# Kernel tuning notes

Hardware: AMD Instinct MI355X
Metric: run time of the kernel (lower is better)

The kernel has to match this reference:

```python
import jax, jax.numpy as jnp
import numpy as np
import math

N_HEADS = 16
D_EMBED = 1024
D_HEAD = D_EMBED // N_HEADS


def setup_inputs() -> dict:
    key = jax.random.key(0)
    ks = jax.random.split(key, 5)
    B, T = 4, 2048
    x = jax.random.normal(ks[0], (B, T, D_EMBED), dtype=jnp.float32)
    s_in = 1.0 / math.sqrt(D_EMBED)
    W_in = jax.random.normal(ks[1], (3 * D_EMBED, D_EMBED), dtype=jnp.float32) * s_in
    b_in = jax.random.normal(ks[2], (3 * D_EMBED,), dtype=jnp.float32) * s_in
    W_out = jax.random.normal(ks[3], (D_EMBED, D_EMBED), dtype=jnp.float32) * s_in
    b_out = jax.random.normal(ks[4], (D_EMBED,), dtype=jnp.float32) * s_in
    return {"x": x, "W_in": W_in, "b_in": b_in, "W_out": W_out, "b_out": b_out,
            "causal_mask": 1}


def reference(x, W_in, b_in, W_out, b_out, causal_mask):
    B, T, C = x.shape
    # in_proj: x @ W_in^T + b_in -> (B,T,3C), chunk into q,k,v
    qkv = jnp.einsum('btc,ec->bte', x, W_in) + b_in
    q, k, v = jnp.split(qkv, 3, axis=-1)
    # (B,T,H,Dh) -> (B,H,T,Dh)
    def heads(t):
        return t.reshape(B, T, N_HEADS, D_HEAD).transpose(0, 2, 1, 3)
    q, k, v = heads(q), heads(k), heads(v)
    scores = jnp.einsum('bhqd,bhkd->bhqk', q, k) / math.sqrt(D_HEAD)
    if causal_mask:
        mask = jnp.triu(jnp.ones((T, T), dtype=bool), k=1)  # True above diagonal
        scores = jnp.where(mask, -jnp.inf, scores)
    attn = jax.nn.softmax(scores, axis=-1)
    out = jnp.einsum('bhqk,bhkd->bhqd', attn, v)
    out = out.transpose(0, 2, 1, 3).reshape(B, T, C)
    out = jnp.einsum('btc,oc->bto', out, W_out) + b_out
    return out
```

## Files before the change

### kernel.cpp

```cpp
#include <hip/hip_runtime.h>
#include <hip/hip_bf16.h>

#define T_SEQ 2048
#define D_EMB 1024
#define NH    16
#define DH    64
#define NB    4
#define MROWS (NB * T_SEQ)
#define QKVN  (3 * D_EMB)

typedef __attribute__((ext_vector_type(8))) short bf16x8;
typedef __attribute__((ext_vector_type(4))) float f32x4;

__device__ __forceinline__ unsigned short f2bf(float f) {
  __hip_bfloat16 h = __float2bfloat16(f);
  return __builtin_bit_cast(unsigned short, h);
}

__device__ __forceinline__ void gload_lds16(const void* g, void* lds) {
  __builtin_amdgcn_global_load_lds(
      (const __attribute__((address_space(1))) void*)g,
      (__attribute__((address_space(3))) void*)lds, 16, 0, 0);
}

__global__ __launch_bounds__(256) void cvt_kernel(const float* __restrict__ in,
                                                  unsigned short* __restrict__ out,
                                                  int n4) {
  for (int i = blockIdx.x * 256 + threadIdx.x; i < n4; i += gridDim.x * 256) {
    const float4 v = reinterpret_cast<const float4*>(in)[i];
    ushort4 o;
    o.x = f2bf(v.x); o.y = f2bf(v.y); o.z = f2bf(v.z); o.w = f2bf(v.w);
    reinterpret_cast<ushort4*>(out)[i] = o;
  }
}

__global__ __launch_bounds__(256) void transposeV(const unsigned short* __restrict__ qkv,
                                                  unsigned short* __restrict__ vt) {
  __shared__ __align__(16) unsigned short Lt[64 * 72];
  const int tid = threadIdx.x;
  const int t0 = blockIdx.x * 64;
  const int bh = blockIdx.y;
  const int b  = bh >> 4;
  const int h  = bh & 15;
  const unsigned short* src = qkv + (size_t)(b * T_SEQ) * QKVN + 2 * D_EMB + h * DH;
#pragma unroll
  for (int g = 0; g < 2; ++g) {
    const int r = (tid >> 3) + g * 32;
    const int c = tid & 7;
    bf16x8 v = *reinterpret_cast<const bf16x8*>(src + (size_t)(t0 + r) * QKVN + c * 8);
    *reinterpret_cast<bf16x8*>(reinterpret_cast<char*>(Lt) + r * 144 + c * 16) = v;
  }
  __syncthreads();
#pragma unroll
  for (int g = 0; g < 2; ++g) {
    const int d  = (tid >> 3) + g * 32;
    const int tc = tid & 7;
    bf16x8 o;
#pragma unroll
    for (int j = 0; j < 8; ++j)
      ((unsigned short*)&o)[j] = Lt[(tc * 8 + j) * 72 + d];
    *reinterpret_cast<bf16x8*>(vt + ((size_t)bh * 64 + d) * T_SEQ + t0 + tc * 8) = o;
  }
}

template <int OUT_BF16>
__global__ __launch_bounds__(256) void gemm_bt(const unsigned short* __restrict__ A,
                                               const unsigned short* __restrict__ Bt,
                                               const float* __restrict__ bias,
                                               void* __restrict__ Cout,
                                               int M, int N, int K) {
  __shared__ __align__(16) unsigned short As[128 * 64];
  __shared__ __align__(16) unsigned short Bs[128 * 64];

  const int tid = threadIdx.x;
  const int w  = tid >> 6;
  const int l  = tid & 63;
  const int lr = l & 15;
  const int lg = l >> 4;

  const int gx   = gridDim.x;
  const int nwg  = gx * gridDim.y;
  const int orig = blockIdx.y * gx + blockIdx.x;
  const int swz  = (orig & 7) * (nwg >> 3) + (orig >> 3);
  const int bm = (swz / gx) * 128;
  const int bn = (swz % gx) * 128;

  const int wr = (w >> 1) * 64;
  const int wc = (w & 1) * 64;

  f32x4 acc[4][4];
#pragma unroll
  for (int i = 0; i < 4; ++i)
#pragma unroll
    for (int j = 0; j < 4; ++j) acc[i][j] = (f32x4){0.f, 0.f, 0.f, 0.f};

  const int cj = (l & 7) ^ (l >> 3);
  const unsigned short* Ab = A + (size_t)(bm + w * 32 + (l >> 3)) * K + cj * 8;
  const unsigned short* Bb = Bt + (size_t)(bn + w * 32 + (l >> 3)) * K + cj * 8;

  for (int kt = 0; kt < K; kt += 64) {
#pragma unroll
    for (int i = 0; i < 4; ++i) {
      gload_lds16(Ab + kt + (size_t)(i * 8) * K, &As[(w * 32 + i * 8) * 64]);
      gload_lds16(Bb + kt + (size_t)(i * 8) * K, &Bs[(w * 32 + i * 8) * 64]);
    }
    __syncthreads();

#pragma unroll
    for (int kk = 0; kk < 2; ++kk) {
      bf16x8 a[4], b[4];
#pragma unroll
      for (int mi = 0; mi < 4; ++mi) {
        const int R = wr + mi * 16 + lr;
        a[mi] = *reinterpret_cast<const bf16x8*>(
            &As[R * 64 + (((kk * 4 + lg) ^ (lr & 7)) << 3)]);
      }
#pragma unroll
      for (int ni = 0; ni < 4; ++ni) {
        const int R = wc + ni * 16 + lr;
        b[ni] = *reinterpret_cast<const bf16x8*>(
            &Bs[R * 64 + (((kk * 4 + lg) ^ (lr & 7)) << 3)]);
      }
#pragma unroll
      for (int mi = 0; mi < 4; ++mi)
#pragma unroll
        for (int ni = 0; ni < 4; ++ni)
          acc[mi][ni] = __builtin_amdgcn_mfma_f32_16x16x32_bf16(a[mi], b[ni], acc[mi][ni], 0, 0, 0);
    }
    __syncthreads();
  }

#pragma unroll
  for (int mi = 0; mi < 4; ++mi)
#pragma unroll
    for (int ni = 0; ni < 4; ++ni)
#pragma unroll
      for (int i = 0; i < 4; ++i) {
        const int row = bm + wr + mi * 16 + lg * 4 + i;
        const int col = bn + wc + ni * 16 + lr;
        const float v = acc[mi][ni][i] + bias[col];
        if (OUT_BF16)
          ((unsigned short*)Cout)[(size_t)row * N + col] = f2bf(v);
        else
          ((float*)Cout)[(size_t)row * N + col] = v;
      }
}

__global__ __launch_bounds__(512, 4) void attn_fwd(const unsigned short* __restrict__ qkv,
                                                   const unsigned short* __restrict__ vt,
                                                   unsigned short* __restrict__ attn_out,
                                                   const int* __restrict__ causal_flag) {
  __shared__ __align__(16) unsigned short Ks[64 * 64];
  __shared__ __align__(16) unsigned short Vt[64 * 64];
  __shared__ __align__(16) unsigned short Ps[8][16 * 64];

  const int tid = threadIdx.x;
  const int w  = tid >> 6;
  const int l  = tid & 63;
  const int lr = l & 15;
  const int lg = l >> 4;
  const int lk = lg * 8;
  const int bx = blockIdx.x;
  const int bh = blockIdx.y;
  const int b  = bh >> 4;
  const int h  = bh & 15;
  const int causal = causal_flag[0];

  const unsigned short* Qp  = qkv + (size_t)(b * T_SEQ) * QKVN + h * DH;
  const unsigned short* Kp  = Qp + D_EMB;
  const unsigned short* Vtp = vt + (size_t)bh * 64 * T_SEQ;

  const int scj = (l & 7) ^ (l >> 3);
  const int srr = l >> 3;

  for (int qq = 0; qq < 2; ++qq) {
    const int qt = qq ? (15 - bx) : bx;
    const int qbase = qt * 128;
    const int wrow0 = qbase + w * 16;

    bf16x8 qf[2];
#pragma unroll
    for (int ks = 0; ks < 2; ++ks) {
      bf16x8 v = *reinterpret_cast<const bf16x8*>(
          Qp + (size_t)(wrow0 + lr) * QKVN + ks * 32 + lk);
#pragma unroll
      for (int j = 0; j < 8; ++j) {
        const float f = __builtin_bit_cast(float, ((unsigned)(unsigned short)v[j]) << 16)
                        * 0.180336879f;
        v[j] = (short)(__builtin_bit_cast(unsigned, f) >> 16);
      }
      qf[ks] = v;
    }

    f32x4 oacc[4];
    float mrow = -INFINITY, lsum = 0.f;
#pragma unroll
    for (int di = 0; di < 4; ++di) oacc[di] = (f32x4){0.f, 0.f, 0.f, 0.f};

    const int nt = causal ? (qt * 2 + 2) : (T_SEQ / 64);

    for (int kb = 0; kb < nt; ++kb) {
      const int kbase = kb * 64;
      gload_lds16(Kp + (size_t)(kbase + w * 8 + srr) * QKVN + scj * 8,
                  &Ks[(w * 8) * 64]);
      gload_lds16(Vtp + (size_t)(w * 8 + srr) * T_SEQ + kbase + scj * 8,
                  &Vt[(w * 8) * 64]);
      __syncthreads();

      const bool live = !causal || (kbase <= wrow0 + 15);
      if (live) {
        f32x4 s[4];
#pragma unroll
        for (int ni = 0; ni < 4; ++ni) s[ni] = (f32x4){0.f, 0.f, 0.f, 0.f};
#pragma unroll
        for (int ks = 0; ks < 2; ++ks) {
          bf16x8 kf[4];
#pragma unroll
          for (int ni = 0; ni < 4; ++ni) {
            const int R = ni * 16 + lr;
            kf[ni] = *reinterpret_cast<const bf16x8*>(
                &Ks[R * 64 + (((ks * 4 + lg) ^ (lr & 7)) << 3)]);
          }
#pragma unroll
          for (int ni = 0; ni < 4; ++ni)
            s[ni] = __builtin_amdgcn_mfma_f32_16x16x32_bf16(kf[ni], qf[ks], s[ni], 0, 0, 0);
        }

        const bool mm = causal && (kbase + 63 > wrow0);
        const int qrow_rel = wrow0 + lr - kbase;
        float rmax = -INFINITY;
#pragma unroll
        for (int ni = 0; ni < 4; ++ni)
#pragma unroll
          for (int i = 0; i < 4; ++i) {
            float v = s[ni][i];
            if (mm && (ni * 16 + lg * 4 + i > qrow_rel)) v = -INFINITY;
            s[ni][i] = v;
            rmax = fmaxf(rmax, v);
          }
        rmax = fmaxf(rmax, __shfl_xor(rmax, 16));
        rmax = fmaxf(rmax, __shfl_xor(rmax, 32));
        const float mnew = fmaxf(mrow, rmax);
        const float alpha = exp2f(mrow - mnew);
        mrow = mnew;
        float psum = 0.f;
#pragma unroll
        for (int ni = 0; ni < 4; ++ni)
#pragma unroll
          for (int i = 0; i < 4; ++i) {
            const float p = exp2f(s[ni][i] - mnew);
            s[ni][i] = p;
            psum += p;
          }
        psum += __shfl_xor(psum, 16);
        psum += __shfl_xor(psum, 32);
        lsum = lsum * alpha + psum;

#pragma unroll
        for (int i = 0; i < 4; ++i) {
          const float a_bc = __shfl(alpha, (l & 48) | (lg * 4 + i));
#pragma unroll
          for (int di = 0; di < 4; ++di) oacc[di][i] *= a_bc;
        }

#pragma unroll
        for (int ni = 0; ni < 4; ++ni) {
          const unsigned lo = (unsigned)f2bf(s[ni][0]) | ((unsigned)f2bf(s[ni][1]) << 16);
          const unsigned hi = (unsigned)f2bf(s[ni][2]) | ((unsigned)f2bf(s[ni][3]) << 16);
          const int chunk = (ni * 2 + (lg >> 1)) ^ (lr & 7);
          uint2* dst = reinterpret_cast<uint2*>(
              reinterpret_cast<char*>(&Ps[w][0]) + lr * 128 + chunk * 16 + (lg & 1) * 8);
          *dst = make_uint2(lo, hi);
        }

#pragma unroll
        for (int ks2 = 0; ks2 < 2; ++ks2) {
          bf16x8 pf, vf[4];
          pf = *reinterpret_cast<const bf16x8*>(
              &Ps[w][lr * 64 + (((ks2 * 4 + lg) ^ (lr & 7)) << 3)]);
#pragma unroll
          for (int di = 0; di < 4; ++di) {
            const int R = di * 16 + lr;
            vf[di] = *reinterpret_cast<const bf16x8*>(
                &Vt[R * 64 + (((ks2 * 4 + lg) ^ (lr & 7)) << 3)]);
          }
#pragma unroll
          for (int di = 0; di < 4; ++di)
            oacc[di] = __builtin_amdgcn_mfma_f32_16x16x32_bf16(pf, vf[di], oacc[di], 0, 0, 0);
        }
      }
      __syncthreads();
    }

#pragma unroll
    for (int i = 0; i < 4; ++i) {
      const float ls = __shfl(lsum, (l & 48) | (lg * 4 + i));
      const float inv = 1.0f / ls;
#pragma unroll
      for (int di = 0; di < 4; ++di) {
        const int q = wrow0 + lg * 4 + i;
        const int d = di * 16 + lr;
        attn_out[(size_t)(b * T_SEQ + q) * D_EMB + h * DH + d] =
            f2bf(oacc[di][i] * inv);
      }
    }
  }
}

extern "C" void kernel_launch(void* const* d_in, const int* in_sizes, int n_in,
                              void* d_out, int out_size, void* d_ws, size_t ws_size,
                              hipStream_t stream) {
  const float* x     = (const float*)d_in[0];
  const float* W_in  = (const float*)d_in[1];
  const float* b_in  = (const float*)d_in[2];
  const float* W_out = (const float*)d_in[3];
  const float* b_out = (const float*)d_in[4];
  const int*   causal = (const int*)d_in[5];
  float* out = (float*)d_out;

  char* ws = (char*)d_ws;
  unsigned short* x_bf    = (unsigned short*)(ws);
  unsigned short* vt      = (unsigned short*)(ws);
  unsigned short* win_bf  = (unsigned short*)(ws + 16777216);
  unsigned short* wout_bf = (unsigned short*)(ws + 23068672);
  unsigned short* qkv     = (unsigned short*)(ws + 25165824);
  unsigned short* attn    = (unsigned short*)(ws + 75497472);

  cvt_kernel<<<2048, 256, 0, stream>>>(x, x_bf, (MROWS * D_EMB) / 4);
  cvt_kernel<<<2048, 256, 0, stream>>>(W_in, win_bf, (QKVN * D_EMB) / 4);
  cvt_kernel<<<1024, 256, 0, stream>>>(W_out, wout_bf, (D_EMB * D_EMB) / 4);

  gemm_bt<1><<<dim3(QKVN / 128, MROWS / 128), 256, 0, stream>>>(
      x_bf, win_bf, b_in, qkv, MROWS, QKVN, D_EMB);

  transposeV<<<dim3(T_SEQ / 64, NB * NH), 256, 0, stream>>>(qkv, vt);

  attn_fwd<<<dim3(8, NB * NH), 512, 0, stream>>>(qkv, vt, attn, causal);

  gemm_bt<0><<<dim3(D_EMB / 128, MROWS / 128), 256, 0, stream>>>(
      attn, wout_bf, b_out, out, MROWS, D_EMB, D_EMB);
}
```

Baseline: 296.3 us.

## Fuse both causal query tiles into one KV pass and skip unneeded rescales

Each block now processes its two paired query tiles (bx and 15-bx) together in a single KV loop. Every K/V tile is loaded into LDS once and shared by both, instead of running two separate sequential passes that reload the early tiles. It also adds a lazy max-rescale: the running max and output rescale are updated only when some row's new max exceeds the old one by more than 8 (log2 units). This costs extra registers for the second accumulator set and Q fragments, which may lower occupancy.

Result: slower. 339.0 us (+14.4%).

```diff
diff --git a/kernel.cpp b/kernel.cpp
--- a/kernel.cpp
+++ b/kernel.cpp
@@ -151,7 +151,7 @@
                                                    unsigned short* __restrict__ attn_out,
                                                    const int* __restrict__ causal_flag) {
   __shared__ __align__(16) unsigned short Ks[64 * 64];
-  __shared__ __align__(16) unsigned short Vt[64 * 64];
+  __shared__ __align__(16) unsigned short Vs[64 * 64];
   __shared__ __align__(16) unsigned short Ps[8][16 * 64];
 
   const int tid = threadIdx.x;
@@ -173,135 +173,161 @@
   const int scj = (l & 7) ^ (l >> 3);
   const int srr = l >> 3;
 
-  for (int qq = 0; qq < 2; ++qq) {
-    const int qt = qq ? (15 - bx) : bx;
-    const int qbase = qt * 128;
-    const int wrow0 = qbase + w * 16;
-
-    bf16x8 qf[2];
-#pragma unroll
-    for (int ks = 0; ks < 2; ++ks) {
+  const int qtA = bx, qtB = 15 - bx;
+  const int wrowA = qtA * 128 + w * 16;
+  const int wrowB = qtB * 128 + w * 16;
+
+  bf16x8 qfA[2], qfB[2];
+#pragma unroll
+  for (int ks = 0; ks < 2; ++ks) {
+#pragma unroll
+    for (int g = 0; g < 2; ++g) {
+      const int wr0 = g ? wrowB : wrowA;
       bf16x8 v = *reinterpret_cast<const bf16x8*>(
-          Qp + (size_t)(wrow0 + lr) * QKVN + ks * 32 + lk);
+          Qp + (size_t)(wr0 + lr) * QKVN + ks * 32 + lk);
 #pragma unroll
       for (int j = 0; j < 8; ++j) {
         const float f = __builtin_bit_cast(float, ((unsigned)(unsigned short)v[j]) << 16)
                         * 0.180336879f;
         v[j] = (short)(__builtin_bit_cast(unsigned, f) >> 16);
       }
-      qf[ks] = v;
-    }
-
-    f32x4 oacc[4];
-    float mrow = -INFINITY, lsum = 0.f;
-#pragma unroll
-    for (int di = 0; di < 4; ++di) oacc[di] = (f32x4){0.f, 0.f, 0.f, 0.f};
-
-    const int nt = causal ? (qt * 2 + 2) : (T_SEQ / 64);
-
-    for (int kb = 0; kb < nt; ++kb) {
-      const int kbase = kb * 64;
-      gload_lds16(Kp + (size_t)(kbase + w * 8 + srr) * QKVN + scj * 8,
-                  &Ks[(w * 8) * 64]);
-      gload_lds16(Vtp + (size_t)(w * 8 + srr) * T_SEQ + kbase + scj * 8,
-                  &Vt[(w * 8) * 64]);
-      __syncthreads();
-
-      const bool live = !causal || (kbase <= wrow0 + 15);
-      if (live) {
-        f32x4 s[4];
-#pragma unroll
-        for (int ni = 0; ni < 4; ++ni) s[ni] = (f32x4){0.f, 0.f, 0.f, 0.f};
-#pragma unroll
-        for (int ks = 0; ks < 2; ++ks) {
-          bf16x8 kf[4];
-#pragma unroll
-          for (int ni = 0; ni < 4; ++ni) {
-            const int R = ni * 16 + lr;
-            kf[ni] = *reinterpret_cast<const bf16x8*>(
-                &Ks[R * 64 + (((ks * 4 + lg) ^ (lr & 7)) << 3)]);
-          }
-#pragma unroll
-          for (int ni = 0; ni < 4; ++ni)
-            s[ni] = __builtin_amdgcn_mfma_f32_16x16x32_bf16(kf[ni], qf[ks], s[ni], 0, 0, 0);
-        }
-
-        const bool mm = causal && (kbase + 63 > wrow0);
-        const int qrow_rel = wrow0 + lr - kbase;
-        float rmax = -INFINITY;
+      if (g) qfB[ks] = v; else qfA[ks] = v;
+    }
+  }
+
+  f32x4 oaccA[4], oaccB[4];
+  float mA = -INFINITY, lA = 0.f, mB = -INFINITY, lB = 0.f;
+#pragma unroll
+  for (int di = 0; di < 4; ++di) {
+    oaccA[di] = (f32x4){0.f, 0.f, 0.f, 0.f};
+    oaccB[di] = (f32x4){0.f, 0.f, 0.f, 0.f};
+  }
+
+  const int nt = causal ? (2 * qtB + 2) : (T_SEQ / 64);
+
+  auto softmax_pv = [&](f32x4 (&s)[4], float& mrow, float& lsum, f32x4 (&oacc)[4],
+                        const int wrow0, const int kbase) {
+    const bool mm = causal && (kbase + 63 > wrow0);
+    if (mm) {
+      const int qrow_rel = wrow0 + lr - kbase;
+#pragma unroll
+      for (int ni = 0; ni < 4; ++ni)
+#pragma unroll
+        for (int i = 0; i < 4; ++i)
+          if (ni * 16 + lg * 4 + i > qrow_rel) s[ni][i] = -INFINITY;
+    }
+    float pmax = -INFINITY;
+#pragma unroll
+    for (int ni = 0; ni < 4; ++ni)
+#pragma unroll
+      for (int i = 0; i < 4; ++i) pmax = fmaxf(pmax, s[ni][i]);
+    pmax = fmaxf(pmax, __shfl_xor(pmax, 16));
+    pmax = fmaxf(pmax, __shfl_xor(pmax, 32));
+    if (!__all(pmax <= mrow + 8.f)) {
+      const float mnew = fmaxf(mrow, pmax);
+      const float alpha = exp2f(mrow - mnew);
+      lsum *= alpha;
+      mrow = mnew;
+#pragma unroll
+      for (int i = 0; i < 4; ++i) {
+        const float a_bc = __shfl(alpha, (l & 48) | (lg * 4 + i));
+#pragma unroll
+        for (int di = 0; di < 4; ++di) oacc[di][i] *= a_bc;
+      }
+    }
+    float psum = 0.f;
+#pragma unroll
+    for (int ni = 0; ni < 4; ++ni)
+#pragma unroll
+      for (int i = 0; i < 4; ++i) {
+        const float p = exp2f(s[ni][i] - mrow);
+        s[ni][i] = p;
+        psum += p;
+      }
+    psum += __shfl_xor(psum, 16);
+    psum += __shfl_xor(psum, 32);
+    lsum += psum;
+#pragma unroll
+    for (int ni = 0; ni < 4; ++ni) {
+      const unsigned lo = (unsigned)f2bf(s[ni][0]) | ((unsigned)f2bf(s[ni][1]) << 16);
+      const unsigned hi = (unsigned)f2bf(s[ni][2]) | ((unsigned)f2bf(s[ni][3]) << 16);
+      const int chunk = (ni * 2 + (lg >> 1)) ^ (lr & 7);
+      uint2* dst = reinterpret_cast<uint2*>(
+          reinterpret_cast<char*>(&Ps[w][0]) + lr * 128 + chunk * 16 + (lg & 1) * 8);
+      *dst = make_uint2(lo, hi);
+    }
+#pragma unroll
+    for (int ks2 = 0; ks2 < 2; ++ks2) {
+      bf16x8 pf, vf[4];
+      pf = *reinterpret_cast<const bf16x8*>(
+          &Ps[w][lr * 64 + (((ks2 * 4 + lg) ^ (lr & 7)) << 3)]);
+#pragma unroll
+      for (int di = 0; di < 4; ++di) {
+        const int R = di * 16 + lr;
+        vf[di] = *reinterpret_cast<const bf16x8*>(
+            &Vs[R * 64 + (((ks2 * 4 + lg) ^ (lr & 7)) << 3)]);
+      }
+#pragma unroll
+      for (int di = 0; di < 4; ++di)
+        oacc[di] = __builtin_amdgcn_mfma_f32_16x16x32_bf16(pf, vf[di], oacc[di], 0, 0, 0);
+    }
+  };
+
+  for (int kb = 0; kb < nt; ++kb) {
+    const int kbase = kb * 64;
+    gload_lds16(Kp + (size_t)(kbase + w * 8 + srr) * QKVN + scj * 8,
+                &Ks[(w * 8) * 64]);
+    gload_lds16(Vtp + (size_t)(w * 8 + srr) * T_SEQ + kbase + scj * 8,
+                &Vs[(w * 8) * 64]);
+    __syncthreads();
+
+    const bool liveA = !causal || (kbase <= wrowA + 15);
+
+    f32x4 sA[4], sB[4];
+#pragma unroll
+    for (int ni = 0; ni < 4; ++ni) {
+      sB[ni] = (f32x4){0.f, 0.f, 0.f, 0.f};
+      sA[ni] = (f32x4){0.f, 0.f, 0.f, 0.f};
+    }
+#pragma unroll
+    for (int ks = 0; ks < 2; ++ks) {
+      bf16x8 kf[4];
+#pragma unroll
+      for (int ni = 0; ni < 4; ++ni) {
+        const int R = ni * 16 + lr;
+        kf[ni] = *reinterpret_cast<const bf16x8*>(
+            &Ks[R * 64 + (((ks * 4 + lg) ^ (lr & 7)) << 3)]);
+      }
+#pragma unroll
+      for (int ni = 0; ni < 4; ++ni)
+        sB[ni] = __builtin_amdgcn_mfma_f32_16x16x32_bf16(kf[ni], qfB[ks], sB[ni], 0, 0, 0);
+      if (liveA) {
 #pragma unroll
         for (int ni = 0; ni < 4; ++ni)
-#pragma unroll
-          for (int i = 0; i < 4; ++i) {
-            float v = s[ni][i];
-            if (mm && (ni * 16 + lg * 4 + i > qrow_rel)) v = -INFINITY;
-            s[ni][i] = v;
-            rmax = fmaxf(rmax, v);
-          }
-        rmax = fmaxf(rmax, __shfl_xor(rmax, 16));
-        rmax = fmaxf(rmax, __shfl_xor(rmax, 32));
-        const float mnew = fmaxf(mrow, rmax);
-        const float alpha = exp2f(mrow - mnew);
-        mrow = mnew;
-        float psum = 0.f;
-#pragma unroll
-        for (int ni = 0; ni < 4; ++ni)
-#pragma unroll
-          for (int i = 0; i < 4; ++i) {
-            const float p = exp2f(s[ni][i] - mnew);
-            s[ni][i] = p;
-            psum += p;
-          }
-        psum += __shfl_xor(psum, 16);
-        psum += __shfl_xor(psum, 32);
-        lsum = lsum * alpha + psum;
-
-#pragma unroll
-        for (int i = 0; i < 4; ++i) {
-          const float a_bc = __shfl(alpha, (l & 48) | (lg * 4 + i));
-#pragma unroll
-          for (int di = 0; di < 4; ++di) oacc[di][i] *= a_bc;
-        }
-
-#pragma unroll
-        for (int ni = 0; ni < 4; ++ni) {
-          const unsigned lo = (unsigned)f2bf(s[ni][0]) | ((unsigned)f2bf(s[ni][1]) << 16);
-          const unsigned hi = (unsigned)f2bf(s[ni][2]) | ((unsigned)f2bf(s[ni][3]) << 16);
-          const int chunk = (ni * 2 + (lg >> 1)) ^ (lr & 7);
-          uint2* dst = reinterpret_cast<uint2*>(
-              reinterpret_cast<char*>(&Ps[w][0]) + lr * 128 + chunk * 16 + (lg & 1) * 8);
-          *dst = make_uint2(lo, hi);
-        }
-
-#pragma unroll
-        for (int ks2 = 0; ks2 < 2; ++ks2) {
-          bf16x8 pf, vf[4];
-          pf = *reinterpret_cast<const bf16x8*>(
-              &Ps[w][lr * 64 + (((ks2 * 4 + lg) ^ (lr & 7)) << 3)]);
-#pragma unroll
-          for (int di = 0; di < 4; ++di) {
-            const int R = di * 16 + lr;
-            vf[di] = *reinterpret_cast<const bf16x8*>(
-                &Vt[R * 64 + (((ks2 * 4 + lg) ^ (lr & 7)) << 3)]);
-          }
-#pragma unroll
-          for (int di = 0; di < 4; ++di)
-            oacc[di] = __builtin_amdgcn_mfma_f32_16x16x32_bf16(pf, vf[di], oacc[di], 0, 0, 0);
-        }
-      }
-      __syncthreads();
-    }
-
+          sA[ni] = __builtin_amdgcn_mfma_f32_16x16x32_bf16(kf[ni], qfA[ks], sA[ni], 0, 0, 0);
+      }
+    }
+
+    softmax_pv(sB, mB, lB, oaccB, wrowB, kbase);
+    if (liveA) softmax_pv(sA, mA, lA, oaccA, wrowA, kbase);
+
+    __syncthreads();
+  }
+
+#pragma unroll
+  for (int g = 0; g < 2; ++g) {
+    const int wr0 = g ? wrowB : wrowA;
+    const float lsum = g ? lB : lA;
 #pragma unroll
     for (int i = 0; i < 4; ++i) {
       const float ls = __shfl(lsum, (l & 48) | (lg * 4 + i));
       const float inv = 1.0f / ls;
 #pragma unroll
       for (int di = 0; di < 4; ++di) {
-        const int q = wrow0 + lg * 4 + i;
+        const int q = wr0 + lg * 4 + i;
         const int d = di * 16 + lr;
-        attn_out[(size_t)(b * T_SEQ + q) * D_EMB + h * DH + d] =
-            f2bf(oacc[di][i] * inv);
+        const f32x4& oa = g ? oaccB[di] : oaccA[di];
+        attn_out[(size_t)(b * T_SEQ + q) * D_EMB + h * DH + d] = f2bf(oa[i] * inv);
       }
     }
   }
```
